# Kernel tuning notes

Hardware: AMD Instinct MI355X
Metric: run time of the kernel (lower is better)

Reference implementation:

```python
import jax, jax.numpy as jnp
import numpy as np

D_MODEL = 512
NUM_HEADS = 8
DEPTH = D_MODEL // NUM_HEADS
EPS = 1e-08


def _phi(x):
    # feature map: elu(x) + 1 (strictly positive, as in 'Transformers are RNNs')
    return jax.nn.elu(x) + 1.0


def setup_inputs() -> dict:
    key = jax.random.key(0)
    ks = jax.random.split(key, 9)
    B, S = 4, 8192
    scale = 1.0 / np.sqrt(D_MODEL)
    return {
        "q": jax.random.normal(ks[0], (B, S, D_MODEL), jnp.float32),
        "k": jax.random.normal(ks[1], (B, S, D_MODEL), jnp.float32),
        "v": jax.random.normal(ks[2], (B, S, D_MODEL), jnp.float32),
        "wq": jax.random.normal(ks[3], (D_MODEL, D_MODEL), jnp.float32) * scale,
        "bq": jnp.zeros((D_MODEL,), jnp.float32),
        "wk": jax.random.normal(ks[4], (D_MODEL, D_MODEL), jnp.float32) * scale,
        "bk": jnp.zeros((D_MODEL,), jnp.float32),
        "wv": jax.random.normal(ks[5], (D_MODEL, D_MODEL), jnp.float32) * scale,
        "bv": jnp.zeros((D_MODEL,), jnp.float32),
    }


def reference(q, k, v, wq, bq, wk, bk, wv, bv):
    B, S, _ = q.shape
    # projections
    qp = q @ wq + bq
    kp = k @ wk + bk
    vp = v @ wv + bv
    # split heads -> [B, S, H, D]
    qh = _phi(qp.reshape(B, S, NUM_HEADS, DEPTH))
    kh = _phi(kp.reshape(B, S, NUM_HEADS, DEPTH))
    vh = vp.reshape(B, S, NUM_HEADS, DEPTH)
    # kv state: [B, D, E, H]
    kv = jnp.einsum('bshd,bshe->bdeh', kh, vh)
    # normalizer
    k_red = jnp.sum(kh, axis=1) + EPS                    # [B, H, D]
    z = 1.0 / jnp.einsum('blhd,bhd->blh', qh, k_red)     # [B, L, H]
    out = jnp.einsum('blhd,bdeh,blh->blhe', qh, kv, z)   # [B, L, H, E]
    return out.reshape(B, S, NUM_HEADS * DEPTH)
```

## Files before the change

kernel.cpp:

```cpp
#include <hip/hip_runtime.h>
#include <hip/hip_bf16.h>

#define DM 512
#define HEADS 8
#define DEPTH 64
#define BATCH 4
#define SEQ 8192
#define MROWS (BATCH*SEQ)

using short8 = __attribute__((ext_vector_type(8))) short;
using floatx4 = __attribute__((ext_vector_type(4))) float;

#define AS1 __attribute__((address_space(1)))
#define AS3 __attribute__((address_space(3)))

static __device__ __forceinline__ float bf2f(unsigned short u) {
    union { unsigned int i; float f; } x; x.i = ((unsigned int)u) << 16; return x.f;
}
static __device__ __forceinline__ unsigned short f2bf(float f) {
    union { float f; unsigned int i; } x; x.f = f;
    unsigned int i = x.i;
    return (unsigned short)((i + 0x7FFFu + ((i >> 16) & 1u)) >> 16);
}
static __device__ __forceinline__ unsigned int pack2(float a, float b) {
    return (unsigned int)f2bf(a) | ((unsigned int)f2bf(b) << 16);
}
static __device__ __forceinline__ unsigned int pack2_rtz(float a, float b) {
    union { float f; unsigned int u; } x, y; x.f = a; y.f = b;
    return (x.u >> 16) | (y.u & 0xFFFF0000u);
}
static __device__ __forceinline__ void gl_lds16(const unsigned short* g, unsigned short* l) {
    __builtin_amdgcn_global_load_lds((const AS1 unsigned int*)g, (AS3 unsigned int*)l, 16, 0, 0);
}

__global__ __launch_bounds__(256) void wprep_kernel(const float* __restrict__ wq,
                                                    const float* __restrict__ wk,
                                                    const float* __restrict__ wv,
                                                    unsigned short* __restrict__ wqT,
                                                    unsigned short* __restrict__ wkT,
                                                    unsigned short* __restrict__ wvT) {
    const float* w = blockIdx.y == 0 ? wq : (blockIdx.y == 1 ? wk : wv);
    unsigned short* wT = blockIdx.y == 0 ? wqT : (blockIdx.y == 1 ? wkT : wvT);
    int idx = blockIdx.x * 256 + threadIdx.x;
    int k = idx & (DM - 1);
    int n = idx >> 9;
    wT[n * DM + k] = f2bf(w[k * DM + n]);
}

__global__ __launch_bounds__(256) void proj3_kernel(
        const float* __restrict__ q, const float* __restrict__ k, const float* __restrict__ v,
        const unsigned short* __restrict__ wqT, const unsigned short* __restrict__ wkT,
        const unsigned short* __restrict__ wvT,
        const float* __restrict__ bq, const float* __restrict__ bk, const float* __restrict__ bv,
        unsigned short* __restrict__ qh, unsigned short* __restrict__ kh,
        unsigned short* __restrict__ vh) {
    __shared__ unsigned short As[64][72];
    __shared__ unsigned short Bs[256 * 64];

    const int t = threadIdx.x;
    const int w = t >> 6;
    const int l15 = t & 15;
    const int g = (t >> 4) & 3;

    const int which = blockIdx.y;
    const float* X = which == 0 ? q : (which == 1 ? k : v);
    const unsigned short* WT = which == 0 ? wqT : (which == 1 ? wkT : wvT);
    const float* bias = which == 0 ? bq : (which == 1 ? bk : bv);
    unsigned short* Y = which == 0 ? qh : (which == 1 ? kh : vh);
    const bool phi = (which < 2);

    const int flat = blockIdx.x;
    const int wg = (flat & 7) * 128 + (flat >> 3);
    const int m0 = (wg >> 1) * 64;
    const int n0 = (wg & 1) * 256;
    const int wc = w * 64;

    const int arow0 = t >> 3;
    const int arow1 = 32 + arow0;
    const int acol = (t & 7) * 8;
    const float* xp0 = X + (size_t)(m0 + arow0) * DM + acol;
    const float* xp1 = X + (size_t)(m0 + arow1) * DM + acol;

    const unsigned short* gb[8];
    unsigned short* lb[8];
    #pragma unroll
    for (int i = 0; i < 8; ++i) {
        int c = i * 256 + t;
        int r = c >> 3;
        int gd = (c & 7) ^ (r & 7);
        gb[i] = WT + (size_t)(n0 + r) * DM + gd * 8;
        lb[i] = Bs + ((size_t)i * 256 + w * 64) * 8;
    }

    float bvx[4];
    #pragma unroll
    for (int n = 0; n < 4; ++n) bvx[n] = bias[n0 + wc + n * 16 + l15];

    floatx4 acc[4][4] = {};
    float4 av0, av1, av2, av3;
    av0 = *(const float4*)xp0; av1 = *(const float4*)(xp0 + 4);
    av2 = *(const float4*)xp1; av3 = *(const float4*)(xp1 + 4);

    #pragma unroll 1
    for (int tile = 0; tile < 8; ++tile) {
        __syncthreads();
        const int koff = tile * 64;
        #pragma unroll
        for (int i = 0; i < 8; ++i) gl_lds16(gb[i] + koff, lb[i]);
        *(uint4*)&As[arow0][acol] = make_uint4(pack2_rtz(av0.x, av0.y), pack2_rtz(av0.z, av0.w),
                                               pack2_rtz(av1.x, av1.y), pack2_rtz(av1.z, av1.w));
        *(uint4*)&As[arow1][acol] = make_uint4(pack2_rtz(av2.x, av2.y), pack2_rtz(av2.z, av2.w),
                                               pack2_rtz(av3.x, av3.y), pack2_rtz(av3.z, av3.w));
        if (tile < 7) {
            av0 = *(const float4*)(xp0 + koff + 64); av1 = *(const float4*)(xp0 + koff + 68);
            av2 = *(const float4*)(xp1 + koff + 64); av3 = *(const float4*)(xp1 + koff + 68);
        }
        __syncthreads();
        #pragma unroll
        for (int kk = 0; kk < 2; ++kk) {
            short8 af[4], bfr[4];
            #pragma unroll
            for (int m = 0; m < 4; ++m)
                af[m] = *(const short8*)&As[m * 16 + l15][kk * 32 + g * 8];
            #pragma unroll
            for (int n = 0; n < 4; ++n) {
                int r = wc + n * 16 + l15;
                int ch = (kk * 4 + g) ^ (r & 7);
                bfr[n] = *(const short8*)&Bs[r * 64 + ch * 8];
            }
            #pragma unroll
            for (int m = 0; m < 4; ++m)
                #pragma unroll
                for (int n = 0; n < 4; ++n)
                    acc[m][n] = __builtin_amdgcn_mfma_f32_16x16x32_bf16(af[m], bfr[n], acc[m][n], 0, 0, 0);
        }
    }

    #pragma unroll
    for (int n = 0; n < 4; ++n) {
        int col = n0 + wc + n * 16 + l15;
        float bb = bvx[n];
        #pragma unroll
        for (int m = 0; m < 4; ++m) {
            #pragma unroll
            for (int j = 0; j < 4; ++j) {
                int row = m0 + m * 16 + g * 4 + j;
                float val = acc[m][n][j] + bb;
                if (phi) val = (val > 0.0f) ? (val + 1.0f) : __expf(val);
                Y[(size_t)row * DM + col] = f2bf(val);
            }
        }
    }
}

#define KV_CHUNK 256
#define KV_TILE 32
__global__ __launch_bounds__(256) void kv_kernel(const unsigned short* __restrict__ kh,
                                                 const unsigned short* __restrict__ vh,
                                                 float* __restrict__ kv,
                                                 float* __restrict__ kred) {
    __shared__ unsigned short khT[64][40];
    __shared__ unsigned short vhT[64][40];

    const int t = threadIdx.x;
    const int w = t >> 6;
    const int l15 = t & 15;
    const int g = (t >> 4) & 3;
    const int b = blockIdx.z, h = blockIdx.y;
    const int s0 = blockIdx.x * KV_CHUNK;

    const int s_i = t >> 3;
    const int d0 = (t & 7) * 8;

    const size_t gbase = ((size_t)b * SEQ + s0 + s_i) * DM + h * DEPTH + d0;

    short8 ones;
    #pragma unroll
    for (int i = 0; i < 8; ++i) ones[i] = (short)0x3F80;

    floatx4 acc[5] = {};

    int4 kr = *(const int4*)(kh + gbase);
    int4 vr = *(const int4*)(vh + gbase);

    #pragma unroll
    for (int tile = 0; tile < KV_CHUNK / KV_TILE; ++tile) {
        {
            const unsigned short* kk = (const unsigned short*)&kr;
            const unsigned short* vv = (const unsigned short*)&vr;
            #pragma unroll
            for (int i = 0; i < 8; ++i) khT[d0 + i][s_i] = kk[i];
            #pragma unroll
            for (int i = 0; i < 8; ++i) vhT[d0 + i][s_i] = vv[i];
        }
        if (tile + 1 < KV_CHUNK / KV_TILE) {
            size_t off = gbase + (size_t)(tile + 1) * KV_TILE * DM;
            kr = *(const int4*)(kh + off);
            vr = *(const int4*)(vh + off);
        }
        __syncthreads();

        short8 af = *(const short8*)&khT[w * 16 + l15][g * 8];
        short8 bf0 = *(const short8*)&vhT[0 * 16 + l15][g * 8];
        short8 bf1 = *(const short8*)&vhT[1 * 16 + l15][g * 8];
        short8 bf2 = *(const short8*)&vhT[2 * 16 + l15][g * 8];
        short8 bf3 = *(const short8*)&vhT[3 * 16 + l15][g * 8];
        acc[0] = __builtin_amdgcn_mfma_f32_16x16x32_bf16(af, bf0, acc[0], 0, 0, 0);
        acc[1] = __builtin_amdgcn_mfma_f32_16x16x32_bf16(af, bf1, acc[1], 0, 0, 0);
        acc[2] = __builtin_amdgcn_mfma_f32_16x16x32_bf16(af, bf2, acc[2], 0, 0, 0);
        acc[3] = __builtin_amdgcn_mfma_f32_16x16x32_bf16(af, ones, acc[3], 0, 0, 0);
        acc[4] = __builtin_amdgcn_mfma_f32_16x16x32_bf16(af, bf3, acc[4], 0, 0, 0);
        __syncthreads();
    }

    float* kvp = kv + (size_t)(b * HEADS + h) * (DEPTH * DEPTH);
    #pragma unroll
    for (int j = 0; j < 4; ++j) {
        int drow = w * 16 + g * 4 + j;
        atomicAdd(&kvp[drow * DEPTH + 0 * 16 + l15], acc[0][j]);
        atomicAdd(&kvp[drow * DEPTH + 1 * 16 + l15], acc[1][j]);
        atomicAdd(&kvp[drow * DEPTH + 2 * 16 + l15], acc[2][j]);
        atomicAdd(&kvp[drow * DEPTH + 3 * 16 + l15], acc[4][j]);
    }
    if (l15 == 0) {
        float* krp = kred + (b * HEADS + h) * DEPTH;
        #pragma unroll
        for (int j = 0; j < 4; ++j)
            atomicAdd(&krp[w * 16 + g * 4 + j], acc[3][j]);
    }
}

__global__ __launch_bounds__(256) void out_kernel(const unsigned short* __restrict__ qh,
                                                  const float* __restrict__ kv,
                                                  const float* __restrict__ kred,
                                                  float* __restrict__ out) {
    __shared__ unsigned short Qs[256 * 64];
    __shared__ unsigned short KVTs[80][72];

    const int t = threadIdx.x;
    const int l = t & 63;
    const int w = t >> 6;
    const int l15 = l & 15;
    const int g = l >> 4;
    const int b = blockIdx.z, h = blockIdx.y;
    const int s0 = blockIdx.x * 256;
    const int wr = w * 64;

    const size_t qbase = ((size_t)b * SEQ + s0) * DM + h * DEPTH;
    #pragma unroll
    for (int i = 0; i < 8; ++i) {
        int c = i * 256 + t;
        int r = c >> 3;
        int gp = c & 7;
        int gd = gp ^ (r & 7);
        const unsigned short* gsrc = qh + qbase + (size_t)r * DM + gd * 8;
        unsigned short* ldst = Qs + ((size_t)i * 256 + w * 64) * 8;
        gl_lds16(gsrc, ldst);
    }

    const float* kvp = kv + (size_t)(b * HEADS + h) * (DEPTH * DEPTH);
    const float* krp = kred + (size_t)(b * HEADS + h) * DEPTH;
    #pragma unroll
    for (int j = 0; j < 20; ++j) {
        int f = j * 256 + t;
        int e = f >> 6, d = f & 63;
        float val = (e < 64) ? kvp[d * DEPTH + e]
                  : (e == 64 ? (krp[d] + 1e-8f) : 0.0f);
        KVTs[e][d] = f2bf(val);
    }

    __syncthreads();

    short8 af[2][4], bfr[2][5];
    #pragma unroll
    for (int kk = 0; kk < 2; ++kk) {
        #pragma unroll
        for (int m = 0; m < 4; ++m) {
            int r = wr + m * 16 + l15;
            int ch = (kk * 4 + g) ^ (r & 7);
            af[kk][m] = *(const short8*)(Qs + r * 64 + ch * 8);
        }
        #pragma unroll
        for (int n = 0; n < 5; ++n)
            bfr[kk][n] = *(const short8*)&KVTs[n * 16 + l15][kk * 32 + g * 8];
    }

    floatx4 acc[4][5] = {};
    #pragma unroll
    for (int kk = 0; kk < 2; ++kk)
        #pragma unroll
        for (int m = 0; m < 4; ++m)
            #pragma unroll
            for (int n = 0; n < 5; ++n)
                acc[m][n] = __builtin_amdgcn_mfma_f32_16x16x32_bf16(af[kk][m], bfr[kk][n], acc[m][n], 0, 0, 0);

    float* op = out + ((size_t)b * SEQ + s0) * DM + h * DEPTH;
    #pragma unroll
    for (int m = 0; m < 4; ++m) {
        #pragma unroll
        for (int j = 0; j < 4; ++j) {
            float den = __shfl(acc[m][4][j], l & 48);
            float z = 1.0f / den;
            int row = wr + m * 16 + g * 4 + j;
            #pragma unroll
            for (int n = 0; n < 4; ++n)
                op[(size_t)row * DM + n * 16 + l15] = acc[m][n][j] * z;
        }
    }
}

extern "C" void kernel_launch(void* const* d_in, const int* in_sizes, int n_in,
                              void* d_out, int out_size, void* d_ws, size_t ws_size,
                              hipStream_t stream) {
    const float* q  = (const float*)d_in[0];
    const float* k  = (const float*)d_in[1];
    const float* v  = (const float*)d_in[2];
    const float* wq = (const float*)d_in[3];
    const float* bq = (const float*)d_in[4];
    const float* wk = (const float*)d_in[5];
    const float* bk = (const float*)d_in[6];
    const float* wv = (const float*)d_in[7];
    const float* bv = (const float*)d_in[8];
    float* out = (float*)d_out;

    char* ws = (char*)d_ws;
    const size_t sz_h = (size_t)MROWS * DM * 2;
    unsigned short* qh  = (unsigned short*)(ws);
    unsigned short* kh  = (unsigned short*)(ws + sz_h);
    unsigned short* vh  = (unsigned short*)(ws + 2 * sz_h);
    unsigned short* wqT = (unsigned short*)(ws + 3 * sz_h);
    unsigned short* wkT = wqT + DM * DM;
    unsigned short* wvT = wkT + DM * DM;
    float* kvbuf   = (float*)(ws + 3 * sz_h + (size_t)3 * DM * DM * 2);
    float* kredbuf = kvbuf + BATCH * HEADS * DEPTH * DEPTH;

    hipMemsetAsync(kvbuf, 0,
                   (size_t)(BATCH * HEADS * DEPTH * DEPTH + BATCH * HEADS * DEPTH) * sizeof(float),
                   stream);

    wprep_kernel<<<dim3(DM * DM / 256, 3), 256, 0, stream>>>(wq, wk, wv, wqT, wkT, wvT);

    proj3_kernel<<<dim3(1024, 3), 256, 0, stream>>>(q, k, v, wqT, wkT, wvT,
                                                    bq, bk, bv, qh, kh, vh);

    kv_kernel<<<dim3(SEQ / KV_CHUNK, HEADS, BATCH), 256, 0, stream>>>(kh, vh, kvbuf, kredbuf);
    out_kernel<<<dim3(SEQ / 256, HEADS, BATCH), 256, 0, stream>>>(qh, kvbuf, kredbuf, out);
}
```

Measured before the change: 191.1 us.

## Enlarge projection GEMM tile to 128x256 with 512-thread workgroups

The projection kernel now computes a 128-row by 256-column output tile per workgroup with 8 waves arranged 2x4, instead of a 64x256 tile with 4 waves. Each staged tile of transposed bf16 weights in LDS is reused by twice as many rows, which halves weight traffic per output and halves the grid size. The cost is higher LDS use and bigger workgroups, which may lower occupancy and leave fewer workgroups to fill the GPU. An unused packing helper is also removed.

```diff
diff --git a/kernel.cpp b/kernel.cpp
--- a/kernel.cpp
+++ b/kernel.cpp
@@ -21,9 +21,6 @@
     union { float f; unsigned int i; } x; x.f = f;
     unsigned int i = x.i;
     return (unsigned short)((i + 0x7FFFu + ((i >> 16) & 1u)) >> 16);
-}
-static __device__ __forceinline__ unsigned int pack2(float a, float b) {
-    return (unsigned int)f2bf(a) | ((unsigned int)f2bf(b) << 16);
 }
 static __device__ __forceinline__ unsigned int pack2_rtz(float a, float b) {
     union { float f; unsigned int u; } x, y; x.f = a; y.f = b;
@@ -47,14 +44,14 @@
     wT[n * DM + k] = f2bf(w[k * DM + n]);
 }
 
-__global__ __launch_bounds__(256) void proj3_kernel(
+__global__ __launch_bounds__(512) void proj3_kernel(
         const float* __restrict__ q, const float* __restrict__ k, const float* __restrict__ v,
         const unsigned short* __restrict__ wqT, const unsigned short* __restrict__ wkT,
         const unsigned short* __restrict__ wvT,
         const float* __restrict__ bq, const float* __restrict__ bk, const float* __restrict__ bv,
         unsigned short* __restrict__ qh, unsigned short* __restrict__ kh,
         unsigned short* __restrict__ vh) {
-    __shared__ unsigned short As[64][72];
+    __shared__ unsigned short As[128][72];
     __shared__ unsigned short Bs[256 * 64];
 
     const int t = threadIdx.x;
@@ -70,26 +67,25 @@
     const bool phi = (which < 2);
 
     const int flat = blockIdx.x;
-    const int wg = (flat & 7) * 128 + (flat >> 3);
-    const int m0 = (wg >> 1) * 64;
+    const int wg = (flat & 7) * 64 + (flat >> 3);
+    const int m0 = (wg >> 1) * 128;
     const int n0 = (wg & 1) * 256;
-    const int wc = w * 64;
-
-    const int arow0 = t >> 3;
-    const int arow1 = 32 + arow0;
-    const int acol = (t & 7) * 8;
-    const float* xp0 = X + (size_t)(m0 + arow0) * DM + acol;
-    const float* xp1 = X + (size_t)(m0 + arow1) * DM + acol;
-
-    const unsigned short* gb[8];
-    unsigned short* lb[8];
-    #pragma unroll
-    for (int i = 0; i < 8; ++i) {
-        int c = i * 256 + t;
+    const int wr = (w >> 2) * 64;
+    const int wc = (w & 3) * 64;
+
+    const int arow = t >> 2;
+    const int aq16 = (t & 3) * 16;
+    const float* xp = X + (size_t)(m0 + arow) * DM + aq16;
+
+    const unsigned short* gb[4];
+    unsigned short* lb[4];
+    #pragma unroll
+    for (int i = 0; i < 4; ++i) {
+        int c = i * 512 + t;
         int r = c >> 3;
         int gd = (c & 7) ^ (r & 7);
         gb[i] = WT + (size_t)(n0 + r) * DM + gd * 8;
-        lb[i] = Bs + ((size_t)i * 256 + w * 64) * 8;
+        lb[i] = Bs + ((size_t)i * 512 + w * 64) * 8;
     }
 
     float bvx[4];
@@ -98,22 +94,22 @@
 
     floatx4 acc[4][4] = {};
     float4 av0, av1, av2, av3;
-    av0 = *(const float4*)xp0; av1 = *(const float4*)(xp0 + 4);
-    av2 = *(const float4*)xp1; av3 = *(const float4*)(xp1 + 4);
+    av0 = *(const float4*)xp;        av1 = *(const float4*)(xp + 4);
+    av2 = *(const float4*)(xp + 8);  av3 = *(const float4*)(xp + 12);
 
     #pragma unroll 1
     for (int tile = 0; tile < 8; ++tile) {
         __syncthreads();
         const int koff = tile * 64;
         #pragma unroll
-        for (int i = 0; i < 8; ++i) gl_lds16(gb[i] + koff, lb[i]);
-        *(uint4*)&As[arow0][acol] = make_uint4(pack2_rtz(av0.x, av0.y), pack2_rtz(av0.z, av0.w),
-                                               pack2_rtz(av1.x, av1.y), pack2_rtz(av1.z, av1.w));
-        *(uint4*)&As[arow1][acol] = make_uint4(pack2_rtz(av2.x, av2.y), pack2_rtz(av2.z, av2.w),
-                                               pack2_rtz(av3.x, av3.y), pack2_rtz(av3.z, av3.w));
+        for (int i = 0; i < 4; ++i) gl_lds16(gb[i] + koff, lb[i]);
+        *(uint4*)&As[arow][aq16] = make_uint4(pack2_rtz(av0.x, av0.y), pack2_rtz(av0.z, av0.w),
+                                              pack2_rtz(av1.x, av1.y), pack2_rtz(av1.z, av1.w));
+        *(uint4*)&As[arow][aq16 + 8] = make_uint4(pack2_rtz(av2.x, av2.y), pack2_rtz(av2.z, av2.w),
+                                                  pack2_rtz(av3.x, av3.y), pack2_rtz(av3.z, av3.w));
         if (tile < 7) {
-            av0 = *(const float4*)(xp0 + koff + 64); av1 = *(const float4*)(xp0 + koff + 68);
-            av2 = *(const float4*)(xp1 + koff + 64); av3 = *(const float4*)(xp1 + koff + 68);
+            av0 = *(const float4*)(xp + koff + 64); av1 = *(const float4*)(xp + koff + 68);
+            av2 = *(const float4*)(xp + koff + 72); av3 = *(const float4*)(xp + koff + 76);
         }
         __syncthreads();
         #pragma unroll
@@ -121,7 +117,7 @@
             short8 af[4], bfr[4];
             #pragma unroll
             for (int m = 0; m < 4; ++m)
-                af[m] = *(const short8*)&As[m * 16 + l15][kk * 32 + g * 8];
+                af[m] = *(const short8*)&As[wr + m * 16 + l15][kk * 32 + g * 8];
             #pragma unroll
             for (int n = 0; n < 4; ++n) {
                 int r = wc + n * 16 + l15;
@@ -144,7 +140,7 @@
         for (int m = 0; m < 4; ++m) {
             #pragma unroll
             for (int j = 0; j < 4; ++j) {
-                int row = m0 + m * 16 + g * 4 + j;
+                int row = m0 + wr + m * 16 + g * 4 + j;
                 float val = acc[m][n][j] + bb;
                 if (phi) val = (val > 0.0f) ? (val + 1.0f) : __expf(val);
                 Y[(size_t)row * DM + col] = f2bf(val);
@@ -340,8 +336,8 @@
 
     wprep_kernel<<<dim3(DM * DM / 256, 3), 256, 0, stream>>>(wq, wk, wv, wqT, wkT, wvT);
 
-    proj3_kernel<<<dim3(1024, 3), 256, 0, stream>>>(q, k, v, wqT, wkT, wvT,
-                                                    bq, bk, bv, qh, kh, vh);
+    proj3_kernel<<<dim3(512, 3), 512, 0, stream>>>(q, k, v, wqT, wkT, wvT,
+                                                   bq, bk, bv, qh, kh, vh);
 
     kv_kernel<<<dim3(SEQ / KV_CHUNK, HEADS, BATCH), 256, 0, stream>>>(kh, vh, kvbuf, kredbuf);
     out_kernel<<<dim3(SEQ / 256, HEADS, BATCH), 256, 0, stream>>>(qh, kvbuf, kredbuf, out);
```

After: 199.5 us. 4.4% more time.
